# Performance work log

Measured on AMD Instinct MI355X. Metric: run time of the kernel, lower is better.

The kernel has to match this reference:

```python
import jax, jax.numpy as jnp
import numpy as np

N = 50000      # nodes
E = 800000     # edges (before self-loops)
IN = 256       # in_dim
HID = 64       # hidden_dim per head
HEADS = 4
OUT = 256      # out_dim
NEG_SLOPE = 0.2


def setup_inputs() -> dict:
    key = jax.random.key(0)
    ks = jax.random.split(key, 12)
    s = 0.1
    return {
        "x": jax.random.normal(ks[0], (N, IN), jnp.float32),
        "edge_index": jax.random.randint(ks[1], (2, E), 0, N, dtype=jnp.int32),
        # layer 1: GATConv(IN, HID, heads=HEADS, concat=True)
        "W1": jax.random.normal(ks[2], (IN, HEADS * HID), jnp.float32) * s,
        "att_src1": jax.random.normal(ks[3], (HEADS, HID), jnp.float32) * s,
        "att_dst1": jax.random.normal(ks[4], (HEADS, HID), jnp.float32) * s,
        "b1": jnp.zeros((HEADS * HID,), jnp.float32),
        # layer 2: GATConv(HEADS*HID, OUT, heads=1, concat=False)
        "W2": jax.random.normal(ks[5], (HEADS * HID, OUT), jnp.float32) * s,
        "att_src2": jax.random.normal(ks[6], (1, OUT), jnp.float32) * s,
        "att_dst2": jax.random.normal(ks[7], (1, OUT), jnp.float32) * s,
        "b2": jnp.zeros((OUT,), jnp.float32),
    }


def _gat_layer(x, src, dst, W, a_src, a_dst, b, heads, concat):
    n = x.shape[0]
    h = (x @ W).reshape(n, heads, -1)                     # [N,H,F]
    al_s = jnp.einsum('nhf,hf->nh', h, a_src)             # [N,H]
    al_d = jnp.einsum('nhf,hf->nh', h, a_dst)
    e = jax.nn.leaky_relu(al_s[src] + al_d[dst], NEG_SLOPE)  # [E,H]
    # segment softmax over incoming edges of each dst node
    m = jax.lax.stop_gradient(jax.ops.segment_max(e, dst, num_segments=n))
    ex = jnp.exp(e - m[dst])
    denom = jax.ops.segment_sum(ex, dst, num_segments=n)
    alpha = ex / (denom[dst] + 1e-16)                     # [E,H]
    out = jax.ops.segment_sum(h[src] * alpha[:, :, None], dst, num_segments=n)  # [N,H,F]
    out = out.reshape(n, -1) if concat else out.mean(axis=1)
    return out + b


def reference(x, edge_index, W1, att_src1, att_dst1, b1, W2, att_src2, att_dst2, b2):
    n = x.shape[0]
    loop = jnp.arange(n, dtype=edge_index.dtype)
    ei = jnp.concatenate([edge_index, jnp.stack([loop, loop])], axis=1)  # add self loops
    src, dst = ei[0], ei[1]
    h = _gat_layer(x, src, dst, W1, att_src1, att_dst1, b1, HEADS, True)
    h = jax.nn.elu(h)
    out = _gat_layer(h, src, dst, W2, att_src2, att_dst2, b2, 1, False)
    return out
```

## Files before the change

### kernel.cpp

```cpp
#include <hip/hip_runtime.h>
#include <math.h>

#define IN_DIM 256
#define FDIM 256
#define HEADS 4
#define NEG 0.2f
#define MAXD 96

typedef __attribute__((ext_vector_type(8))) short bf16x8;
typedef __attribute__((ext_vector_type(8))) unsigned short u16x8;
typedef __attribute__((ext_vector_type(4))) float f32x4;

__device__ __forceinline__ float leaky(float x){ return x > 0.f ? x : NEG * x; }

__device__ __forceinline__ unsigned short f2bf(float f){
  unsigned int u = __float_as_uint(f);
  unsigned int r = u + 0x7fffu + ((u >> 16) & 1u);
  return (unsigned short)(r >> 16);
}
__device__ __forceinline__ float bf2f(unsigned short s){
  return __uint_as_float(((unsigned int)s) << 16);
}

__device__ __forceinline__ float4 bcast4(float4 v){
  return make_float4(__shfl(v.x,0,64), __shfl(v.y,0,64), __shfl(v.z,0,64), __shfl(v.w,0,64));
}
__device__ __forceinline__ float comp4(float4 v, int h){
  return h==0 ? v.x : h==1 ? v.y : h==2 ? v.z : v.w;
}

__device__ __forceinline__ void gld_lds16(const void* g, void* l){
  __builtin_amdgcn_global_load_lds((const __attribute__((address_space(1))) unsigned int*)g,
                                   (__attribute__((address_space(3))) unsigned int*)l, 16, 0, 0);
}

__global__ void k_hist(const int* __restrict__ dst, int* deg, int E){
  int e = blockIdx.x * blockDim.x + threadIdx.x;
  if (e < E) atomicAdd(&deg[dst[e]], 1);
}

__global__ void k_scanA(const int* __restrict__ deg, int* tmp, int* partials, int n){
  __shared__ int sm[256];
  int i = blockIdx.x * 256 + threadIdx.x;
  int v = (i < n) ? deg[i] + 1 : 0;
  sm[threadIdx.x] = v; __syncthreads();
  for (int off = 1; off < 256; off <<= 1){
    int x = (threadIdx.x >= off) ? sm[threadIdx.x - off] : 0;
    __syncthreads();
    sm[threadIdx.x] += x;
    __syncthreads();
  }
  if (i < n) tmp[i] = sm[threadIdx.x];
  if (threadIdx.x == 255) partials[blockIdx.x] = sm[255];
}

__global__ void k_scanB(int* partials, int nb){
  __shared__ int sm[1024];
  int t = threadIdx.x;
  int v = (t < nb) ? partials[t] : 0;
  sm[t] = v; __syncthreads();
  for (int off = 1; off < 1024; off <<= 1){
    int x = (t >= off) ? sm[t - off] : 0;
    __syncthreads();
    sm[t] += x;
    __syncthreads();
  }
  if (t < nb) partials[t] = sm[t] - v;
}

__global__ void k_scanC(const int* __restrict__ tmp, const int* __restrict__ deg,
                        const int* __restrict__ partials, int* rowptr, int n){
  int i = blockIdx.x * blockDim.x + threadIdx.x;
  if (i < n){
    int incl = tmp[i] + partials[i >> 8];
    rowptr[i] = incl - (deg[i] + 1);
    if (i == n - 1) rowptr[n] = incl;
  }
}

__global__ void k_fill(const int* __restrict__ src, const int* __restrict__ dst,
                       const int* __restrict__ rowptr, int* fill, int* col, int E, int n){
  int e = blockIdx.x * blockDim.x + threadIdx.x;
  if (e < E + n){
    int s, d;
    if (e < E){ s = src[e]; d = dst[e]; } else { s = d = e - E; }
    int pos = atomicAdd(&fill[d], 1);
    col[rowptr[d] + pos] = s;
  }
}

__global__ void k_castwt(const float* __restrict__ x, unsigned short* __restrict__ xb, int M, int castBlocks,
                         const float* __restrict__ W1, unsigned short* __restrict__ W1t,
                         const float* __restrict__ W2, unsigned short* __restrict__ W2t){
  int b = blockIdx.x;
  if (b < castBlocks){
    int idx = b * 256 + threadIdx.x;
    int row = idx >> 6;
    float4 v = make_float4(0.f, 0.f, 0.f, 0.f);
    if (row < M) v = *(const float4*)(x + (size_t)idx * 4);
    ushort4 o;
    o.x = f2bf(v.x); o.y = f2bf(v.y); o.z = f2bf(v.z); o.w = f2bf(v.w);
    *(ushort4*)(xb + (size_t)idx * 4) = o;
  } else {
    int bb = b - castBlocks;
    const float* W = (bb < 256) ? W1 : W2;
    unsigned short* Wt = (bb < 256) ? W1t : W2t;
    int nn = bb & 255, k = threadIdx.x;
    Wt[nn * 256 + k] = f2bf(W[k * 256 + nn]);
  }
}

__global__ __launch_bounds__(256) void k_gemm(const unsigned short* __restrict__ A,
                                              const unsigned short* __restrict__ Bt,
                                              unsigned short* __restrict__ C,
                                              const float* __restrict__ asrc,
                                              const float* __restrict__ adst,
                                              float* __restrict__ als,
                                              float* __restrict__ ald,
                                              int nRows, int multi){
  __shared__ __align__(16) unsigned short sh[8192];
  unsigned short* As = sh;
  unsigned short* Bs = sh + 4096;
  int tid = threadIdx.x;
  int lane = tid & 63, wave = tid >> 6;
  int rowBase = blockIdx.x * 128, colBase = blockIdx.y * 128;
  int wr = (wave & 1) * 64, wc = (wave >> 1) * 64;

  f32x4 acc[4][4] = {};
  int c0 = tid, c1 = tid + 256;
  int r0 = c0 >> 2, kc0 = (c0 & 3) * 8;
  int r1 = c1 >> 2, kc1 = (c1 & 3) * 8;
  int m0 = lane & 15, kq = (lane >> 4) * 8;

  for (int k0 = 0; k0 < 256; k0 += 32){
    gld_lds16(A  + (size_t)(rowBase + r0) * 256 + k0 + kc0, (char*)As + c0 * 16);
    gld_lds16(A  + (size_t)(rowBase + r1) * 256 + k0 + kc1, (char*)As + c1 * 16);
    gld_lds16(Bt + (size_t)(colBase + r0) * 256 + k0 + kc0, (char*)Bs + c0 * 16);
    gld_lds16(Bt + (size_t)(colBase + r1) * 256 + k0 + kc1, (char*)Bs + c1 * 16);
    __syncthreads();
    bf16x8 af[4], bfr[4];
    #pragma unroll
    for (int it = 0; it < 4; ++it)
      af[it] = *(const bf16x8*)(As + (wr + it * 16 + m0) * 32 + kq);
    #pragma unroll
    for (int jt = 0; jt < 4; ++jt)
      bfr[jt] = *(const bf16x8*)(Bs + (wc + jt * 16 + m0) * 32 + kq);
    #pragma unroll
    for (int it = 0; it < 4; ++it)
      #pragma unroll
      for (int jt = 0; jt < 4; ++jt)
        acc[it][jt] = __builtin_amdgcn_mfma_f32_16x16x32_bf16(af[it], bfr[jt], acc[it][jt], 0, 0, 0);
    __syncthreads();
  }
  int cq = lane >> 4, cm = lane & 15;
  int sg = tid & 7;
  float accS[4] = {0.f,0.f,0.f,0.f}, accD[4] = {0.f,0.f,0.f,0.f};
  #pragma unroll
  for (int p = 0; p < 2; ++p){
    if ((wave >> 1) == p){
      #pragma unroll
      for (int it = 0; it < 4; ++it)
        #pragma unroll
        for (int jt = 0; jt < 4; ++jt)
          #pragma unroll
          for (int r = 0; r < 4; ++r)
            sh[(wr + it * 16 + cq * 4 + r) * 64 + jt * 16 + cm] = f2bf(acc[it][jt][r]);
    }
    __syncthreads();
    const float* asl = asrc + colBase + p * 64 + sg * 8;
    const float* adl = adst + colBase + p * 64 + sg * 8;
    float as8[8], ad8[8];
    #pragma unroll
    for (int k = 0; k < 8; ++k){ as8[k] = asl[k]; ad8[k] = adl[k]; }
    #pragma unroll
    for (int q = 0; q < 4; ++q){
      int id = tid + q * 256;
      int r = id >> 3;
      u16x8 v = *(const u16x8*)(sh + r * 64 + sg * 8);
      *(u16x8*)(C + (size_t)(rowBase + r) * 256 + colBase + p * 64 + sg * 8) = v;
      float ps = 0.f, pd = 0.f;
      #pragma unroll
      for (int k = 0; k < 8; ++k){
        float hv = bf2f((unsigned short)v[k]);
        ps += hv * as8[k]; pd += hv * ad8[k];
      }
      if (multi){
        #pragma unroll
        for (int off = 4; off >= 1; off >>= 1){
          ps += __shfl_down(ps, off, 8);
          pd += __shfl_down(pd, off, 8);
        }
        if (sg == 0){
          int grow = rowBase + r;
          if (grow < nRows){
            int hp = (colBase >> 6) + p;
            als[(size_t)grow * 4 + hp] = ps;
            ald[(size_t)grow * 4 + hp] = pd;
          }
        }
      } else {
        accS[q] += ps; accD[q] += pd;
      }
    }
    __syncthreads();
  }
  if (!multi){
    #pragma unroll
    for (int q = 0; q < 4; ++q){
      float ps = accS[q], pd = accD[q];
      #pragma unroll
      for (int off = 4; off >= 1; off >>= 1){
        ps += __shfl_down(ps, off, 8);
        pd += __shfl_down(pd, off, 8);
      }
      if (sg == 0){
        int r = (tid + q * 256) >> 3;
        int grow = rowBase + r;
        if (grow < nRows){
          atomicAdd(&als[grow], ps);
          atomicAdd(&ald[grow], pd);
        }
      }
    }
  }
}

__global__ __launch_bounds__(256) void k_agg1(const unsigned short* __restrict__ Hb,
    const float* __restrict__ als, const float* __restrict__ ald,
    const int* __restrict__ rowptr, const int* __restrict__ col,
    const float* __restrict__ b, unsigned short* __restrict__ outb, int n){
  __shared__ __align__(16) int   colS[4][MAXD];
  __shared__ __align__(16) float wS[4][MAXD][4];
  int wave = threadIdx.x >> 6, t = threadIdx.x & 63;
  int i = blockIdx.x * 4 + wave; if (i >= n) i = n - 1;
  int start = rowptr[i];
  int deg = rowptr[i + 1] - start;
  float4 adv = *(const float4*)(ald + (size_t)i * 4);
  bool staged = (deg <= MAXD);

  float4 ls = make_float4(0.f, 0.f, 0.f, 0.f);
  if (staged){
    for (int j = t; j < deg; j += 64){
      int s = col[start + j];
      colS[wave][j] = s;
      float4 a = *(const float4*)(als + (size_t)s * 4);
      float4 w = make_float4(__expf(leaky(a.x + adv.x)), __expf(leaky(a.y + adv.y)),
                             __expf(leaky(a.z + adv.z)), __expf(leaky(a.w + adv.w)));
      *(float4*)(&wS[wave][j][0]) = w;
      ls.x += w.x; ls.y += w.y; ls.z += w.z; ls.w += w.w;
    }
  } else {
    for (int j = t; j < deg; j += 64){
      int s = col[start + j];
      float4 a = *(const float4*)(als + (size_t)s * 4);
      ls.x += __expf(leaky(a.x + adv.x)); ls.y += __expf(leaky(a.y + adv.y));
      ls.z += __expf(leaky(a.z + adv.z)); ls.w += __expf(leaky(a.w + adv.w));
    }
  }
  #pragma unroll
  for (int off = 32; off >= 1; off >>= 1) ls = make_float4(
      ls.x + __shfl_down(ls.x, off, 64), ls.y + __shfl_down(ls.y, off, 64),
      ls.z + __shfl_down(ls.z, off, 64), ls.w + __shfl_down(ls.w, off, 64));
  float4 d4 = bcast4(ls);
  __syncthreads();

  int e2 = t >> 5, l32 = t & 31;
  int h = l32 >> 3, f = l32 * 8;
  float inv = 1.f / (comp4(d4, h) + 1e-16f);
  const unsigned short* Hrow = Hb + f;
  float a0[8] = {0,0,0,0,0,0,0,0}, a1[8] = {0,0,0,0,0,0,0,0};
  if (staged){
    int j = 0;
    for (; j + 3 < deg; j += 4){
      int j0 = j + e2, j1 = j + 2 + e2;
      int s0 = colS[wave][j0], s1 = colS[wave][j1];
      float w0 = wS[wave][j0][h], w1 = wS[wave][j1][h];
      u16x8 h0 = *(const u16x8*)(Hrow + (size_t)s0 * FDIM);
      u16x8 h1 = *(const u16x8*)(Hrow + (size_t)s1 * FDIM);
      #pragma unroll
      for (int k = 0; k < 8; ++k){ a0[k] += bf2f(h0[k]) * w0; a1[k] += bf2f(h1[k]) * w1; }
    }
    for (; j < deg; j += 2){
      int jj = j + e2;
      if (jj < deg){
        int s = colS[wave][jj]; float w = wS[wave][jj][h];
        u16x8 hh = *(const u16x8*)(Hrow + (size_t)s * FDIM);
        #pragma unroll
        for (int k = 0; k < 8; ++k) a0[k] += bf2f(hh[k]) * w;
      }
    }
  } else {
    float adh = comp4(adv, h);
    for (int j = e2; j < deg; j += 2){
      int s = col[start + j];
      float w = __expf(leaky(als[(size_t)s * 4 + h] + adh));
      u16x8 hh = *(const u16x8*)(Hrow + (size_t)s * FDIM);
      #pragma unroll
      for (int k = 0; k < 8; ++k) a0[k] += bf2f(hh[k]) * w;
    }
  }
  float r[8];
  #pragma unroll
  for (int k = 0; k < 8; ++k){
    r[k] = a0[k] + a1[k];
    r[k] += __shfl_down(r[k], 32, 64);
  }
  if (t < 32){
    float4 bA = *(const float4*)(b + f);
    float4 bB = *(const float4*)(b + f + 4);
    float bb[8] = {bA.x, bA.y, bA.z, bA.w, bB.x, bB.y, bB.z, bB.w};
    u16x8 o;
    #pragma unroll
    for (int k = 0; k < 8; ++k){
      float v = r[k] * inv + bb[k];
      v = (v > 0.f) ? v : (__expf(v) - 1.f);
      o[k] = f2bf(v);
    }
    *(u16x8*)(outb + (size_t)i * FDIM + f) = o;
  }
}

__global__ __launch_bounds__(256) void k_agg2(const unsigned short* __restrict__ Hb,
    const float* __restrict__ als, const float* __restrict__ ald,
    const int* __restrict__ rowptr, const int* __restrict__ col,
    const float* __restrict__ b, float* __restrict__ out, int n){
  __shared__ __align__(16) int   colS[4][MAXD];
  __shared__ __align__(16) float wS[4][MAXD];
  int wave = threadIdx.x >> 6, t = threadIdx.x & 63;
  int i = blockIdx.x * 4 + wave; if (i >= n) i = n - 1;
  int start = rowptr[i];
  int deg = rowptr[i + 1] - start;
  float adv = ald[i];
  bool staged = (deg <= MAXD);

  float ls = 0.f;
  if (staged){
    for (int j = t; j < deg; j += 64){
      int s = col[start + j];
      colS[wave][j] = s;
      float w = __expf(leaky(als[s] + adv));
      wS[wave][j] = w;
      ls += w;
    }
  } else {
    for (int j = t; j < deg; j += 64) ls += __expf(leaky(als[col[start + j]] + adv));
  }
  #pragma unroll
  for (int off = 32; off >= 1; off >>= 1) ls += __shfl_down(ls, off, 64);
  float inv = 1.f / (__shfl(ls, 0, 64) + 1e-16f);
  __syncthreads();

  int e2 = t >> 5, l32 = t & 31;
  int f = l32 * 8;
  const unsigned short* Hrow = Hb + f;
  float a0[8] = {0,0,0,0,0,0,0,0}, a1[8] = {0,0,0,0,0,0,0,0};
  if (staged){
    int j = 0;
    for (; j + 3 < deg; j += 4){
      int j0 = j + e2, j1 = j + 2 + e2;
      int s0 = colS[wave][j0], s1 = colS[wave][j1];
      float w0 = wS[wave][j0], w1 = wS[wave][j1];
      u16x8 h0 = *(const u16x8*)(Hrow + (size_t)s0 * FDIM);
      u16x8 h1 = *(const u16x8*)(Hrow + (size_t)s1 * FDIM);
      #pragma unroll
      for (int k = 0; k < 8; ++k){ a0[k] += bf2f(h0[k]) * w0; a1[k] += bf2f(h1[k]) * w1; }
    }
    for (; j < deg; j += 2){
      int jj = j + e2;
      if (jj < deg){
        int s = colS[wave][jj]; float w = wS[wave][jj];
        u16x8 hh = *(const u16x8*)(Hrow + (size_t)s * FDIM);
        #pragma unroll
        for (int k = 0; k < 8; ++k) a0[k] += bf2f(hh[k]) * w;
      }
    }
  } else {
    for (int j = e2; j < deg; j += 2){
      int s = col[start + j];
      float w = __expf(leaky(als[s] + adv));
      u16x8 hh = *(const u16x8*)(Hrow + (size_t)s * FDIM);
      #pragma unroll
      for (int k = 0; k < 8; ++k) a0[k] += bf2f(hh[k]) * w;
    }
  }
  float r[8];
  #pragma unroll
  for (int k = 0; k < 8; ++k){
    r[k] = a0[k] + a1[k];
    r[k] += __shfl_down(r[k], 32, 64);
  }
  if (t < 32){
    float4 bA = *(const float4*)(b + f);
    float4 bB = *(const float4*)(b + f + 4);
    float4 oA = make_float4(r[0]*inv + bA.x, r[1]*inv + bA.y, r[2]*inv + bA.z, r[3]*inv + bA.w);
    float4 oB = make_float4(r[4]*inv + bB.x, r[5]*inv + bB.y, r[6]*inv + bB.z, r[7]*inv + bB.w);
    *(float4*)(out + (size_t)i * FDIM + f) = oA;
    *(float4*)(out + (size_t)i * FDIM + f + 4) = oB;
  }
}

extern "C" void kernel_launch(void* const* d_in, const int* in_sizes, int n_in,
                              void* d_out, int out_size, void* d_ws, size_t ws_size,
                              hipStream_t stream){
  const float* x   = (const float*)d_in[0];
  const int*   ei  = (const int*)d_in[1];
  const float* W1  = (const float*)d_in[2];
  const float* as1 = (const float*)d_in[3];
  const float* ad1 = (const float*)d_in[4];
  const float* b1  = (const float*)d_in[5];
  const float* W2  = (const float*)d_in[6];
  const float* as2 = (const float*)d_in[7];
  const float* ad2 = (const float*)d_in[8];
  const float* b2  = (const float*)d_in[9];
  float* out = (float*)d_out;

  int n = in_sizes[0] / IN_DIM;
  int E = in_sizes[1] / 2;
  int Mpad = (n + 127) & ~127;
  const int* srcIdx = ei;
  const int* dstIdx = ei + E;

  char* ws = (char*)d_ws;
  size_t off = 0;
  auto alloc = [&](size_t bytes) -> void* {
    void* p = ws + off; off += (bytes + 255) & ~(size_t)255; return p;
  };
  unsigned short* bufA = (unsigned short*)alloc((size_t)Mpad * FDIM * 2);
  unsigned short* bufB = (unsigned short*)alloc((size_t)Mpad * FDIM * 2);
  unsigned short* W1t  = (unsigned short*)alloc(256 * 256 * 2);
  unsigned short* W2t  = (unsigned short*)alloc(256 * 256 * 2);
  int*   tmp      = (int*)alloc((size_t)n * 4);
  int*   deg      = (int*)alloc((size_t)n * 4);
  int*   fill     = (int*)alloc((size_t)n * 4);
  int*   rowptr   = (int*)alloc((size_t)(n + 1) * 4);
  int*   partials = (int*)alloc(1024 * 4);
  int*   col      = (int*)alloc((size_t)(E + n) * 4);
  float* als1     = (float*)alloc((size_t)n * HEADS * 4);
  float* ald1     = (float*)alloc((size_t)n * HEADS * 4);
  float* als2     = (float*)alloc((size_t)n * 4);
  float* ald2     = (float*)alloc((size_t)n * 4);
  (void)ws_size;

  int nb = (n + 255) / 256;
  hipMemsetAsync(deg, 0, (size_t)n * 4, stream);
  hipMemsetAsync(fill, 0, (size_t)n * 4, stream);
  hipMemsetAsync(als2, 0, (size_t)n * 4, stream);
  hipMemsetAsync(ald2, 0, (size_t)n * 4, stream);
  k_hist<<<(E + 255) / 256, 256, 0, stream>>>(dstIdx, deg, E);
  k_scanA<<<nb, 256, 0, stream>>>(deg, tmp, partials, n);
  k_scanB<<<1, 1024, 0, stream>>>(partials, nb);
  k_scanC<<<nb, 256, 0, stream>>>(tmp, deg, partials, rowptr, n);
  k_fill<<<(E + n + 255) / 256, 256, 0, stream>>>(srcIdx, dstIdx, rowptr, fill, col, E, n);

  int castBlocks = (Mpad * (FDIM / 4) + 255) / 256;
  k_castwt<<<castBlocks + 512, 256, 0, stream>>>(x, bufA, n, castBlocks, W1, W1t, W2, W2t);

  dim3 gg(Mpad / 128, FDIM / 128);
  int ga = (n + 3) / 4;
  k_gemm<<<gg, 256, 0, stream>>>(bufA, W1t, bufB, as1, ad1, als1, ald1, n, 1);
  k_agg1<<<ga, 256, 0, stream>>>(bufB, als1, ald1, rowptr, col, b1, bufA, n);
  k_gemm<<<gg, 256, 0, stream>>>(bufA, W2t, bufB, as2, ad2, als2, ald2, n, 0);
  k_agg2<<<ga, 256, 0, stream>>>(bufB, als2, ald2, rowptr, col, b2, out, n);
}
```

Baseline: 408.7 us.

## Store features in 32-column slices and split aggregation into alpha and sliced gather kernels

The GEMM now writes its output as eight column slices, each holding 32 bf16 features per row, and the second GEMM reads its A operand in that sliced layout. Attention coefficients are computed once per edge into a separate alpha buffer. New gather kernels then aggregate one 32-feature slice per block, so each slice array is small enough to stay in cache during the random source-node gathers. This adds alpha write and read traffic, extra kernel launches and eight times as many aggregation blocks, each re-reading col and alpha.

```diff
diff --git a/kernel.cpp b/kernel.cpp
--- a/kernel.cpp
+++ b/kernel.cpp
@@ -5,7 +5,6 @@
 #define FDIM 256
 #define HEADS 4
 #define NEG 0.2f
-#define MAXD 96
 
 typedef __attribute__((ext_vector_type(8))) short bf16x8;
 typedef __attribute__((ext_vector_type(8))) unsigned short u16x8;
@@ -24,9 +23,6 @@
 
 __device__ __forceinline__ float4 bcast4(float4 v){
   return make_float4(__shfl(v.x,0,64), __shfl(v.y,0,64), __shfl(v.z,0,64), __shfl(v.w,0,64));
-}
-__device__ __forceinline__ float comp4(float4 v, int h){
-  return h==0 ? v.x : h==1 ? v.y : h==2 ? v.z : v.w;
 }
 
 __device__ __forceinline__ void gld_lds16(const void* g, void* l){
@@ -117,7 +113,7 @@
                                               const float* __restrict__ adst,
                                               float* __restrict__ als,
                                               float* __restrict__ ald,
-                                              int nRows, int multi){
+                                              int nRows, int multi, int Mpad, int sliceA){
   __shared__ __align__(16) unsigned short sh[8192];
   unsigned short* As = sh;
   unsigned short* Bs = sh + 4096;
@@ -132,9 +128,12 @@
   int r1 = c1 >> 2, kc1 = (c1 & 3) * 8;
   int m0 = lane & 15, kq = (lane >> 4) * 8;
 
+  size_t slicePitch = (size_t)Mpad * 32;
   for (int k0 = 0; k0 < 256; k0 += 32){
-    gld_lds16(A  + (size_t)(rowBase + r0) * 256 + k0 + kc0, (char*)As + c0 * 16);
-    gld_lds16(A  + (size_t)(rowBase + r1) * 256 + k0 + kc1, (char*)As + c1 * 16);
+    const unsigned short* Ak = sliceA ? (A + (size_t)(k0 >> 5) * slicePitch) : (A + k0);
+    size_t rstride = sliceA ? 32 : 256;
+    gld_lds16(Ak + (size_t)(rowBase + r0) * rstride + kc0, (char*)As + c0 * 16);
+    gld_lds16(Ak + (size_t)(rowBase + r1) * rstride + kc1, (char*)As + c1 * 16);
     gld_lds16(Bt + (size_t)(colBase + r0) * 256 + k0 + kc0, (char*)Bs + c0 * 16);
     gld_lds16(Bt + (size_t)(colBase + r1) * 256 + k0 + kc1, (char*)Bs + c1 * 16);
     __syncthreads();
@@ -167,17 +166,19 @@
             sh[(wr + it * 16 + cq * 4 + r) * 64 + jt * 16 + cm] = f2bf(acc[it][jt][r]);
     }
     __syncthreads();
-    const float* asl = asrc + colBase + p * 64 + sg * 8;
-    const float* adl = adst + colBase + p * 64 + sg * 8;
+    int feat = colBase + p * 64 + sg * 8;
+    const float* asl = asrc + feat;
+    const float* adl = adst + feat;
     float as8[8], ad8[8];
     #pragma unroll
     for (int k = 0; k < 8; ++k){ as8[k] = asl[k]; ad8[k] = adl[k]; }
+    size_t cSliceBase = (size_t)(feat >> 5) * slicePitch + (feat & 31);
     #pragma unroll
     for (int q = 0; q < 4; ++q){
       int id = tid + q * 256;
       int r = id >> 3;
       u16x8 v = *(const u16x8*)(sh + r * 64 + sg * 8);
-      *(u16x8*)(C + (size_t)(rowBase + r) * 256 + colBase + p * 64 + sg * 8) = v;
+      *(u16x8*)(C + cSliceBase + (size_t)(rowBase + r) * 32) = v;
       float ps = 0.f, pd = 0.f;
       #pragma unroll
       for (int k = 0; k < 8; ++k){
@@ -225,177 +226,110 @@
   }
 }
 
-__global__ __launch_bounds__(256) void k_agg1(const unsigned short* __restrict__ Hb,
-    const float* __restrict__ als, const float* __restrict__ ald,
+__global__ __launch_bounds__(256) void k_alpha4(const float* __restrict__ als, const float* __restrict__ ald,
     const int* __restrict__ rowptr, const int* __restrict__ col,
-    const float* __restrict__ b, unsigned short* __restrict__ outb, int n){
-  __shared__ __align__(16) int   colS[4][MAXD];
-  __shared__ __align__(16) float wS[4][MAXD][4];
+    float* __restrict__ alpha, int Ep, int n){
   int wave = threadIdx.x >> 6, t = threadIdx.x & 63;
   int i = blockIdx.x * 4 + wave; if (i >= n) i = n - 1;
-  int start = rowptr[i];
-  int deg = rowptr[i + 1] - start;
+  int start = rowptr[i], deg = rowptr[i + 1] - start;
   float4 adv = *(const float4*)(ald + (size_t)i * 4);
-  bool staged = (deg <= MAXD);
-
-  float4 ls = make_float4(0.f, 0.f, 0.f, 0.f);
-  if (staged){
-    for (int j = t; j < deg; j += 64){
-      int s = col[start + j];
-      colS[wave][j] = s;
-      float4 a = *(const float4*)(als + (size_t)s * 4);
-      float4 w = make_float4(__expf(leaky(a.x + adv.x)), __expf(leaky(a.y + adv.y)),
-                             __expf(leaky(a.z + adv.z)), __expf(leaky(a.w + adv.w)));
-      *(float4*)(&wS[wave][j][0]) = w;
-      ls.x += w.x; ls.y += w.y; ls.z += w.z; ls.w += w.w;
-    }
-  } else {
-    for (int j = t; j < deg; j += 64){
-      int s = col[start + j];
-      float4 a = *(const float4*)(als + (size_t)s * 4);
-      ls.x += __expf(leaky(a.x + adv.x)); ls.y += __expf(leaky(a.y + adv.y));
-      ls.z += __expf(leaky(a.z + adv.z)); ls.w += __expf(leaky(a.w + adv.w));
-    }
+  float4 sum = make_float4(0.f, 0.f, 0.f, 0.f);
+  for (int j = t; j < deg; j += 64){
+    int s = col[start + j];
+    float4 a = *(const float4*)(als + (size_t)s * 4);
+    sum.x += __expf(leaky(a.x + adv.x)); sum.y += __expf(leaky(a.y + adv.y));
+    sum.z += __expf(leaky(a.z + adv.z)); sum.w += __expf(leaky(a.w + adv.w));
   }
   #pragma unroll
-  for (int off = 32; off >= 1; off >>= 1) ls = make_float4(
-      ls.x + __shfl_down(ls.x, off, 64), ls.y + __shfl_down(ls.y, off, 64),
-      ls.z + __shfl_down(ls.z, off, 64), ls.w + __shfl_down(ls.w, off, 64));
-  float4 d4 = bcast4(ls);
-  __syncthreads();
-
-  int e2 = t >> 5, l32 = t & 31;
-  int h = l32 >> 3, f = l32 * 8;
-  float inv = 1.f / (comp4(d4, h) + 1e-16f);
-  const unsigned short* Hrow = Hb + f;
-  float a0[8] = {0,0,0,0,0,0,0,0}, a1[8] = {0,0,0,0,0,0,0,0};
-  if (staged){
-    int j = 0;
-    for (; j + 3 < deg; j += 4){
-      int j0 = j + e2, j1 = j + 2 + e2;
-      int s0 = colS[wave][j0], s1 = colS[wave][j1];
-      float w0 = wS[wave][j0][h], w1 = wS[wave][j1][h];
-      u16x8 h0 = *(const u16x8*)(Hrow + (size_t)s0 * FDIM);
-      u16x8 h1 = *(const u16x8*)(Hrow + (size_t)s1 * FDIM);
-      #pragma unroll
-      for (int k = 0; k < 8; ++k){ a0[k] += bf2f(h0[k]) * w0; a1[k] += bf2f(h1[k]) * w1; }
-    }
-    for (; j < deg; j += 2){
-      int jj = j + e2;
-      if (jj < deg){
-        int s = colS[wave][jj]; float w = wS[wave][jj][h];
-        u16x8 hh = *(const u16x8*)(Hrow + (size_t)s * FDIM);
-        #pragma unroll
-        for (int k = 0; k < 8; ++k) a0[k] += bf2f(hh[k]) * w;
-      }
-    }
-  } else {
-    float adh = comp4(adv, h);
-    for (int j = e2; j < deg; j += 2){
-      int s = col[start + j];
-      float w = __expf(leaky(als[(size_t)s * 4 + h] + adh));
-      u16x8 hh = *(const u16x8*)(Hrow + (size_t)s * FDIM);
-      #pragma unroll
-      for (int k = 0; k < 8; ++k) a0[k] += bf2f(hh[k]) * w;
-    }
-  }
-  float r[8];
-  #pragma unroll
-  for (int k = 0; k < 8; ++k){
-    r[k] = a0[k] + a1[k];
-    r[k] += __shfl_down(r[k], 32, 64);
-  }
-  if (t < 32){
-    float4 bA = *(const float4*)(b + f);
-    float4 bB = *(const float4*)(b + f + 4);
-    float bb[8] = {bA.x, bA.y, bA.z, bA.w, bB.x, bB.y, bB.z, bB.w};
-    u16x8 o;
-    #pragma unroll
-    for (int k = 0; k < 8; ++k){
-      float v = r[k] * inv + bb[k];
-      v = (v > 0.f) ? v : (__expf(v) - 1.f);
-      o[k] = f2bf(v);
-    }
-    *(u16x8*)(outb + (size_t)i * FDIM + f) = o;
-  }
-}
-
-__global__ __launch_bounds__(256) void k_agg2(const unsigned short* __restrict__ Hb,
-    const float* __restrict__ als, const float* __restrict__ ald,
+  for (int off = 32; off >= 1; off >>= 1) sum = make_float4(
+      sum.x + __shfl_down(sum.x, off, 64), sum.y + __shfl_down(sum.y, off, 64),
+      sum.z + __shfl_down(sum.z, off, 64), sum.w + __shfl_down(sum.w, off, 64));
+  float4 d4 = bcast4(sum);
+  float4 inv = make_float4(1.f/(d4.x+1e-16f), 1.f/(d4.y+1e-16f), 1.f/(d4.z+1e-16f), 1.f/(d4.w+1e-16f));
+  for (int j = t; j < deg; j += 64){
+    int s = col[start + j];
+    float4 a = *(const float4*)(als + (size_t)s * 4);
+    alpha[0*(size_t)Ep + start + j] = __expf(leaky(a.x + adv.x)) * inv.x;
+    alpha[1*(size_t)Ep + start + j] = __expf(leaky(a.y + adv.y)) * inv.y;
+    alpha[2*(size_t)Ep + start + j] = __expf(leaky(a.z + adv.z)) * inv.z;
+    alpha[3*(size_t)Ep + start + j] = __expf(leaky(a.w + adv.w)) * inv.w;
+  }
+}
+
+__global__ __launch_bounds__(256) void k_alpha1h(const float* __restrict__ als, const float* __restrict__ ald,
     const int* __restrict__ rowptr, const int* __restrict__ col,
-    const float* __restrict__ b, float* __restrict__ out, int n){
-  __shared__ __align__(16) int   colS[4][MAXD];
-  __shared__ __align__(16) float wS[4][MAXD];
+    float* __restrict__ alpha, int n){
   int wave = threadIdx.x >> 6, t = threadIdx.x & 63;
   int i = blockIdx.x * 4 + wave; if (i >= n) i = n - 1;
-  int start = rowptr[i];
-  int deg = rowptr[i + 1] - start;
+  int start = rowptr[i], deg = rowptr[i + 1] - start;
   float adv = ald[i];
-  bool staged = (deg <= MAXD);
-
-  float ls = 0.f;
-  if (staged){
-    for (int j = t; j < deg; j += 64){
-      int s = col[start + j];
-      colS[wave][j] = s;
-      float w = __expf(leaky(als[s] + adv));
-      wS[wave][j] = w;
-      ls += w;
-    }
-  } else {
-    for (int j = t; j < deg; j += 64) ls += __expf(leaky(als[col[start + j]] + adv));
-  }
+  float sum = 0.f;
+  for (int j = t; j < deg; j += 64) sum += __expf(leaky(als[col[start + j]] + adv));
   #pragma unroll
-  for (int off = 32; off >= 1; off >>= 1) ls += __shfl_down(ls, off, 64);
-  float inv = 1.f / (__shfl(ls, 0, 64) + 1e-16f);
-  __syncthreads();
-
-  int e2 = t >> 5, l32 = t & 31;
-  int f = l32 * 8;
-  const unsigned short* Hrow = Hb + f;
-  float a0[8] = {0,0,0,0,0,0,0,0}, a1[8] = {0,0,0,0,0,0,0,0};
-  if (staged){
-    int j = 0;
-    for (; j + 3 < deg; j += 4){
-      int j0 = j + e2, j1 = j + 2 + e2;
-      int s0 = colS[wave][j0], s1 = colS[wave][j1];
-      float w0 = wS[wave][j0], w1 = wS[wave][j1];
-      u16x8 h0 = *(const u16x8*)(Hrow + (size_t)s0 * FDIM);
-      u16x8 h1 = *(const u16x8*)(Hrow + (size_t)s1 * FDIM);
-      #pragma unroll
-      for (int k = 0; k < 8; ++k){ a0[k] += bf2f(h0[k]) * w0; a1[k] += bf2f(h1[k]) * w1; }
-    }
-    for (; j < deg; j += 2){
-      int jj = j + e2;
-      if (jj < deg){
-        int s = colS[wave][jj]; float w = wS[wave][jj];
-        u16x8 hh = *(const u16x8*)(Hrow + (size_t)s * FDIM);
-        #pragma unroll
-        for (int k = 0; k < 8; ++k) a0[k] += bf2f(hh[k]) * w;
-      }
-    }
-  } else {
-    for (int j = e2; j < deg; j += 2){
-      int s = col[start + j];
-      float w = __expf(leaky(als[s] + adv));
-      u16x8 hh = *(const u16x8*)(Hrow + (size_t)s * FDIM);
-      #pragma unroll
-      for (int k = 0; k < 8; ++k) a0[k] += bf2f(hh[k]) * w;
-    }
-  }
-  float r[8];
-  #pragma unroll
-  for (int k = 0; k < 8; ++k){
-    r[k] = a0[k] + a1[k];
-    r[k] += __shfl_down(r[k], 32, 64);
-  }
-  if (t < 32){
-    float4 bA = *(const float4*)(b + f);
-    float4 bB = *(const float4*)(b + f + 4);
-    float4 oA = make_float4(r[0]*inv + bA.x, r[1]*inv + bA.y, r[2]*inv + bA.z, r[3]*inv + bA.w);
-    float4 oB = make_float4(r[4]*inv + bB.x, r[5]*inv + bB.y, r[6]*inv + bB.z, r[7]*inv + bB.w);
-    *(float4*)(out + (size_t)i * FDIM + f) = oA;
-    *(float4*)(out + (size_t)i * FDIM + f + 4) = oB;
+  for (int off = 32; off >= 1; off >>= 1) sum += __shfl_down(sum, off, 64);
+  float inv = 1.f / (__shfl(sum, 0, 64) + 1e-16f);
+  for (int j = t; j < deg; j += 64)
+    alpha[start + j] = __expf(leaky(als[col[start + j]] + adv)) * inv;
+}
+
+__global__ __launch_bounds__(256) void k_gat1(const unsigned short* __restrict__ Hsl,
+    const float* __restrict__ alpha, int Ep,
+    const int* __restrict__ rowptr, const int* __restrict__ col,
+    const float* __restrict__ b, unsigned short* __restrict__ outSl, int n, int Mpad){
+  int s = blockIdx.x & 7, grp = blockIdx.x >> 3;
+  int wave = threadIdx.x >> 6, lane = threadIdx.x & 63;
+  int i = grp * 4 + wave;
+  if (i >= n) return;
+  int start = rowptr[i], deg = rowptr[i + 1] - start;
+  const float* al = alpha + (size_t)(s >> 1) * Ep + start;
+  const unsigned short* Hs = Hsl + (size_t)s * Mpad * 32;
+  int g4 = lane >> 4, l16 = lane & 15;
+  float a0 = 0.f, a1 = 0.f;
+  for (int j = g4; j < deg; j += 4){
+    int src = __builtin_nontemporal_load(col + start + j);
+    float aw = __builtin_nontemporal_load(al + j);
+    unsigned int hv = *(const unsigned int*)(Hs + (size_t)src * 32 + l16 * 2);
+    a0 += aw * bf2f((unsigned short)(hv & 0xffffu));
+    a1 += aw * bf2f((unsigned short)(hv >> 16));
+  }
+  a0 += __shfl_xor(a0, 16); a0 += __shfl_xor(a0, 32);
+  a1 += __shfl_xor(a1, 16); a1 += __shfl_xor(a1, 32);
+  if (lane < 16){
+    float2 bb = *(const float2*)(b + s * 32 + l16 * 2);
+    float v0 = a0 + bb.x, v1 = a1 + bb.y;
+    v0 = (v0 > 0.f) ? v0 : (__expf(v0) - 1.f);
+    v1 = (v1 > 0.f) ? v1 : (__expf(v1) - 1.f);
+    unsigned int o = (unsigned int)f2bf(v0) | ((unsigned int)f2bf(v1) << 16);
+    *(unsigned int*)(outSl + ((size_t)s * Mpad + i) * 32 + l16 * 2) = o;
+  }
+}
+
+__global__ __launch_bounds__(256) void k_gat2(const unsigned short* __restrict__ Hsl,
+    const float* __restrict__ alpha,
+    const int* __restrict__ rowptr, const int* __restrict__ col,
+    const float* __restrict__ b, float* __restrict__ out, int n, int Mpad){
+  int s = blockIdx.x & 7, grp = blockIdx.x >> 3;
+  int wave = threadIdx.x >> 6, lane = threadIdx.x & 63;
+  int i = grp * 4 + wave;
+  if (i >= n) return;
+  int start = rowptr[i], deg = rowptr[i + 1] - start;
+  const float* al = alpha + start;
+  const unsigned short* Hs = Hsl + (size_t)s * Mpad * 32;
+  int g4 = lane >> 4, l16 = lane & 15;
+  float a0 = 0.f, a1 = 0.f;
+  for (int j = g4; j < deg; j += 4){
+    int src = __builtin_nontemporal_load(col + start + j);
+    float aw = __builtin_nontemporal_load(al + j);
+    unsigned int hv = *(const unsigned int*)(Hs + (size_t)src * 32 + l16 * 2);
+    a0 += aw * bf2f((unsigned short)(hv & 0xffffu));
+    a1 += aw * bf2f((unsigned short)(hv >> 16));
+  }
+  a0 += __shfl_xor(a0, 16); a0 += __shfl_xor(a0, 32);
+  a1 += __shfl_xor(a1, 16); a1 += __shfl_xor(a1, 32);
+  if (lane < 16){
+    float2 bb = *(const float2*)(b + s * 32 + l16 * 2);
+    float2 o = make_float2(a0 + bb.x, a1 + bb.y);
+    *(float2*)(out + (size_t)i * FDIM + s * 32 + l16 * 2) = o;
   }
 }
 
@@ -417,6 +351,7 @@
   int n = in_sizes[0] / IN_DIM;
   int E = in_sizes[1] / 2;
   int Mpad = (n + 127) & ~127;
+  int Ep = E + n;
   const int* srcIdx = ei;
   const int* dstIdx = ei + E;
 
@@ -434,11 +369,13 @@
   int*   fill     = (int*)alloc((size_t)n * 4);
   int*   rowptr   = (int*)alloc((size_t)(n + 1) * 4);
   int*   partials = (int*)alloc(1024 * 4);
-  int*   col      = (int*)alloc((size_t)(E + n) * 4);
+  int*   col      = (int*)alloc((size_t)Ep * 4);
   float* als1     = (float*)alloc((size_t)n * HEADS * 4);
   float* ald1     = (float*)alloc((size_t)n * HEADS * 4);
   float* als2     = (float*)alloc((size_t)n * 4);
   float* ald2     = (float*)alloc((size_t)n * 4);
+  float* alpha1   = (float*)alloc((size_t)Ep * HEADS * 4);
+  float* alpha2   = (float*)alloc((size_t)Ep * 4);
   (void)ws_size;
 
   int nb = (n + 255) / 256;
@@ -457,8 +394,11 @@
 
   dim3 gg(Mpad / 128, FDIM / 128);
   int ga = (n + 3) / 4;
-  k_gemm<<<gg, 256, 0, stream>>>(bufA, W1t, bufB, as1, ad1, als1, ald1, n, 1);
-  k_agg1<<<ga, 256, 0, stream>>>(bufB, als1, ald1, rowptr, col, b1, bufA, n);
-  k_gemm<<<gg, 256, 0, stream>>>(bufA, W2t, bufB, as2, ad2, als2, ald2, n, 0);
-  k_agg2<<<ga, 256, 0, stream>>>(bufB, als2, ald2, rowptr, col, b2, out, n);
-}
+  int gGat = ((n + 3) / 4) * 8;
+  k_gemm<<<gg, 256, 0, stream>>>(bufA, W1t, bufB, as1, ad1, als1, ald1, n, 1, Mpad, 0);
+  k_alpha4<<<ga, 256, 0, stream>>>(als1, ald1, rowptr, col, alpha1, Ep, n);
+  k_gat1<<<gGat, 256, 0, stream>>>(bufB, alpha1, Ep, rowptr, col, b1, bufA, n, Mpad);
+  k_gemm<<<gg, 256, 0, stream>>>(bufA, W2t, bufB, as2, ad2, als2, ald2, n, 0, Mpad, 1);
+  k_alpha1h<<<ga, 256, 0, stream>>>(als2, ald2, rowptr, col, alpha2, n);
+  k_gat2<<<gGat, 256, 0, stream>>>(bufB, alpha2, rowptr, col, b2, out, n, Mpad);
+}
```

Measured after the change: 800.6 us. 1.96x slower.
